# Performance work log

Measured on AMD Instinct MI355X. Metric: run time of the kernel, lower is better.

## Reference

```python
import jax, jax.numpy as jnp
import numpy as np

ROPE_THETA = 10000.0
NUM_HEADS = 16


def _apply_rope(t, positions):
    # t: [B, H, S, dh]; positions: [S] int
    dh = t.shape[-1]
    inv_freq = 1.0 / (ROPE_THETA ** (jnp.arange(0, dh, 2, dtype=jnp.float32) / dh))  # [dh/2]
    ang = positions.astype(jnp.float32)[:, None] * inv_freq[None, :]  # [S, dh/2]
    cos = jnp.cos(ang)[None, None]  # [1,1,S,dh/2]
    sin = jnp.sin(ang)[None, None]
    t1 = t[..., 0::2]
    t2 = t[..., 1::2]
    r1 = t1 * cos - t2 * sin
    r2 = t1 * sin + t2 * cos
    # interleave back: (r1_0, r2_0, r1_1, r2_1, ...)
    return jnp.stack([r1, r2], axis=-1).reshape(t.shape)


def setup_inputs() -> dict:
    key = jax.random.key(0)
    ks = jax.random.split(key, 5)
    B, S, D = 4, 2048, 1024
    sigma = np.sqrt(2.0 / (D + D))
    return {
        "x": jax.random.normal(ks[0], (B, S, D), dtype=jnp.float32),
        "WQ": jax.random.normal(ks[1], (D, D), dtype=jnp.float32) * sigma,
        "WK": jax.random.normal(ks[2], (D, D), dtype=jnp.float32) * sigma,
        "WV": jax.random.normal(ks[3], (D, D), dtype=jnp.float32) * sigma,
        "WO": jax.random.normal(ks[4], (D, D), dtype=jnp.float32) * sigma,
        "token_positions": jnp.arange(S, dtype=jnp.int32),
    }


def reference(x, WQ, WK, WV, WO, token_positions):
    B, S, D = x.shape
    H = NUM_HEADS
    dh = D // H

    def proj(W):
        # x @ W.T, then split heads -> [B, H, S, dh]
        return jnp.einsum('bsd,ed->bse', x, W).reshape(B, S, H, dh).transpose(0, 2, 1, 3)

    Q = _apply_rope(proj(WQ), token_positions)
    K = _apply_rope(proj(WK), token_positions)
    V = proj(WV)

    scale = 1.0 / jnp.sqrt(jnp.asarray(dh, dtype=x.dtype))
    scores = jnp.einsum('bhqd,bhkd->bhqk', Q, K) * scale  # [B,H,S,S]
    causal = jnp.tril(jnp.ones((S, S), dtype=bool))
    scores = jnp.where(causal[None, None], scores, jnp.asarray(-jnp.inf, dtype=scores.dtype))
    attn = jax.nn.softmax(scores, axis=-1)
    out = jnp.einsum('bhqk,bhkd->bhqd', attn, V)  # [B,H,S,dh]
    out = out.transpose(0, 2, 1, 3).reshape(B, S, D)
    return out @ WO.T
```

## Files before the change

kernel.cpp:

```cpp
#include <hip/hip_runtime.h>
#include <hip/hip_bf16.h>
#include <math.h>

constexpr int NB   = 4;
constexpr int SEQ  = 2048;
constexpr int DM   = 1024;
constexpr int NH   = 16;
constexpr int DH2  = 64;
constexpr int NROWS = NB * SEQ;

typedef __attribute__((ext_vector_type(8))) short bf16x8;
typedef __attribute__((ext_vector_type(4))) short bf16x4;
typedef __attribute__((ext_vector_type(4))) float f32x4;

__device__ __forceinline__ unsigned short f2bf(float f) {
  __hip_bfloat16 h = __float2bfloat16(f);
  return *reinterpret_cast<unsigned short*>(&h);
}

__device__ __forceinline__ f32x4 mfma16(bf16x8 a, bf16x8 b, f32x4 c) {
  return __builtin_amdgcn_mfma_f32_16x16x32_bf16(a, b, c, 0, 0, 0);
}

__device__ __forceinline__ f32x4 mfma16k16(bf16x4 a, bf16x4 b, f32x4 c) {
  asm("v_mfma_f32_16x16x16_bf16 %0, %1, %2, %0" : "+v"(c) : "v"(a), "v"(b));
  return c;
}

__device__ __forceinline__ void gload_lds16(const void* g, void* l) {
  __builtin_amdgcn_global_load_lds(
      (const __attribute__((address_space(1))) void*)g,
      (__attribute__((address_space(3))) void*)l, 16, 0, 0);
}

__global__ void cast_kernel(const float* __restrict__ in,
                            unsigned short* __restrict__ out, int n4) {
  int i = blockIdx.x * blockDim.x + threadIdx.x;
  int stride = gridDim.x * blockDim.x;
  for (int idx = i; idx < n4; idx += stride) {
    float4 v = reinterpret_cast<const float4*>(in)[idx];
    ushort4 o;
    o.x = f2bf(v.x); o.y = f2bf(v.y); o.z = f2bf(v.z); o.w = f2bf(v.w);
    reinterpret_cast<ushort4*>(out)[idx] = o;
  }
}

__global__ void cast4_kernel(const float* __restrict__ w0, const float* __restrict__ w1,
                             const float* __restrict__ w2, const float* __restrict__ w3,
                             unsigned short* __restrict__ out) {
  constexpr int N4 = DM * DM / 4;
  int idx = blockIdx.x * blockDim.x + threadIdx.x;
  if (idx >= N4) return;
  const float* ins[4] = {w0, w1, w2, w3};
#pragma unroll
  for (int wi = 0; wi < 4; ++wi) {
    float4 v = reinterpret_cast<const float4*>(ins[wi])[idx];
    ushort4 o;
    o.x = f2bf(v.x); o.y = f2bf(v.y); o.z = f2bf(v.z); o.w = f2bf(v.w);
    reinterpret_cast<ushort4*>(out + (size_t)wi * DM * DM)[idx] = o;
  }
}

__global__ void rope_table_kernel(float2* __restrict__ tab, const int* __restrict__ pos) {
  int idx = blockIdx.x * blockDim.x + threadIdx.x;
  if (idx >= SEQ * 32) return;
  int s = idx >> 5, i = idx & 31;
  float inv = powf(10000.0f, -(float)i * (1.0f / 32.0f));
  float ang = (float)pos[s] * inv;
  tab[idx] = make_float2(cosf(ang), sinf(ang));
}

template<int MODE>
__global__ __launch_bounds__(256)
void gemm_bt(const unsigned short* __restrict__ Ag,
             const unsigned short* __restrict__ Bg,
             void* __restrict__ Cout,
             const float2* __restrict__ tab)
{
  constexpr int K = DM;
  __shared__ unsigned short As[128 * 32];
  __shared__ unsigned short Bs[128 * 32];
  const int tid = threadIdx.x;
  const int w = tid >> 6, lane = tid & 63;
  const int wr = w >> 1, wc = w & 1;
  const int r = lane & 15, g = lane >> 4;
  const int rowTile = blockIdx.x, colTile = blockIdx.y;
  const unsigned short* Abase = Ag + (size_t)rowTile * 128 * K;
  const unsigned short* Bbase = Bg + (size_t)colTile * 128 * K;

  f32x4 acc[4][4];
#pragma unroll
  for (int m = 0; m < 4; ++m)
#pragma unroll
    for (int n = 0; n < 4; ++n) acc[m][n] = f32x4{0.f, 0.f, 0.f, 0.f};

  const int e0 = w * 1024 + lane * 8;

  for (int k0 = 0; k0 < K; k0 += 32) {
#pragma unroll
    for (int c = 0; c < 2; ++c) {
      int e = e0 + c * 512;
      int trow = e >> 5, tcol = e & 31;
      gload_lds16(Abase + (size_t)trow * K + k0 + tcol, As + (w * 2 + c) * 512);
      gload_lds16(Bbase + (size_t)trow * K + k0 + tcol, Bs + (w * 2 + c) * 512);
    }
    __syncthreads();
    bf16x8 a[4], b[4];
#pragma unroll
    for (int m = 0; m < 4; ++m)
      a[m] = *reinterpret_cast<const bf16x8*>(As + (wr * 64 + m * 16 + r) * 32 + g * 8);
#pragma unroll
    for (int n = 0; n < 4; ++n)
      b[n] = *reinterpret_cast<const bf16x8*>(Bs + (wc * 64 + n * 16 + r) * 32 + g * 8);
#pragma unroll
    for (int m = 0; m < 4; ++m)
#pragma unroll
      for (int n = 0; n < 4; ++n)
        acc[m][n] = mfma16(a[m], b[n], acc[m][n]);
    __syncthreads();
  }

  const int row0 = rowTile * 128 + wr * 64;
  const int col0 = colTile * 128 + wc * 64;
  if constexpr (MODE == 0) {
    float* C = reinterpret_cast<float*>(Cout);
#pragma unroll
    for (int m = 0; m < 4; ++m)
#pragma unroll
      for (int n = 0; n < 4; ++n)
#pragma unroll
        for (int j = 0; j < 4; ++j) {
          int rr = row0 + m * 16 + g * 4 + j;
          int cc = col0 + n * 16 + r;
          C[(size_t)rr * DM + cc] = acc[m][n][j];
        }
  } else {
    unsigned short* Ob = reinterpret_cast<unsigned short*>(Cout);
#pragma unroll
    for (int m = 0; m < 4; ++m)
#pragma unroll
      for (int n = 0; n < 4; ++n)
#pragma unroll
        for (int j = 0; j < 4; ++j) {
          int rr = row0 + m * 16 + g * 4 + j;
          int ee = col0 + n * 16 + r;
          float val = acc[m][n][j];
          if constexpr (MODE == 1) {
            float partner = __shfl_xor(val, 1);
            int dd = ee & 63;
            int sr = rr & (SEQ - 1);
            float2 cs = tab[sr * 32 + (dd >> 1)];
            val = val * cs.x + (((ee & 1) == 0) ? -partner : partner) * cs.y;
          }
          int bb = rr >> 11;
          int sr2 = rr & (SEQ - 1);
          int h = ee >> 6, d = ee & 63;
          Ob[((size_t)(bb * NH + h) * SEQ + sr2) * DH2 + d] = f2bf(val);
        }
  }
}

__global__ __launch_bounds__(256)
void flash_attn(const unsigned short* __restrict__ Qb,
                const unsigned short* __restrict__ Kb,
                const unsigned short* __restrict__ Vb,
                unsigned short* __restrict__ AO)
{
  constexpr int VST = 68;
  __shared__ unsigned short Kl[2 * 64 * 64];
  __shared__ unsigned short Vt[2][64 * VST];
  const int tid = threadIdx.x;
  const int w = tid >> 6, lane = tid & 63;
  const int r = lane & 15, g = lane >> 4;
  const int pr = blockIdx.x;
  const int bh = blockIdx.y;
  const unsigned short* Qh = Qb + (size_t)bh * SEQ * DH2;
  const unsigned short* Kh = Kb + (size_t)bh * SEQ * DH2;
  const unsigned short* Vh = Vb + (size_t)bh * SEQ * DH2;
  const int bb = bh >> 4, h = bh & 15;
  const int vd  = (lane & 7) * 8;
  const int vkv = w * 16 + (lane >> 3) * 2;
  const float C = 0.18033688f;
  const float M0 = 11.5415603f;
  const float NEG_INF = -__builtin_inff();

  const int krow   = tid >> 3;
  const int kcol16 = (tid & 7) ^ (krow & 7);
  const int kgoff  = krow * 64 + kcol16 * 8;
  const int kread0 = r * 64 + ((g ^ (r & 7)) * 8);
  const int kread1 = r * 64 + (((4 ^ g) ^ (r & 7)) * 8);

  for (int ctx = 0; ctx < 2; ++ctx) {
    const int qt = ctx ? pr : (15 - pr);
    const int q0w = qt * 128 + w * 32;
    const int nT  = 2 * qt + 2;
    const int myT = 2 * qt + 1 + (w >> 1);

    bf16x8 qf[2][2];
#pragma unroll
    for (int mq = 0; mq < 2; ++mq)
#pragma unroll
      for (int kk = 0; kk < 2; ++kk)
        qf[mq][kk] = *reinterpret_cast<const bf16x8*>(
            Qh + (size_t)(q0w + mq * 16 + r) * DH2 + kk * 32 + g * 8);

    gload_lds16(Kh + kgoff, Kl + w * 512);
    gload_lds16(Kh + kgoff + 2048, Kl + 2048 + w * 512);
    {
      uint4 a0 = *reinterpret_cast<const uint4*>(Vh + (size_t)vkv * DH2 + vd);
      uint4 a1 = *reinterpret_cast<const uint4*>(Vh + (size_t)(vkv + 1) * DH2 + vd);
      const unsigned int* d0 = reinterpret_cast<const unsigned int*>(&a0);
      const unsigned int* d1 = reinterpret_cast<const unsigned int*>(&a1);
#pragma unroll
      for (int k2 = 0; k2 < 4; ++k2) {
        *reinterpret_cast<unsigned int*>(&Vt[0][(vd + 2 * k2) * VST + vkv]) =
            __builtin_amdgcn_perm(d1[k2], d0[k2], 0x05040100u);
        *reinterpret_cast<unsigned int*>(&Vt[0][(vd + 2 * k2 + 1) * VST + vkv]) =
            __builtin_amdgcn_perm(d1[k2], d0[k2], 0x07060302u);
      }
    }
    __syncthreads();

    f32x4 oacc[2][4];
    float l_part[2];
#pragma unroll
    for (int mq = 0; mq < 2; ++mq) {
#pragma unroll
      for (int nd = 0; nd < 4; ++nd) oacc[mq][nd] = f32x4{0.f, 0.f, 0.f, 0.f};
      l_part[mq] = 0.f;
    }

    uint4 va0, va1;
    for (int t = 0; t < nT; ++t) {
      const int cur = t & 1;
      const unsigned short* Klp = Kl + (cur ? 4096 : 0);
      unsigned short* Kln = Kl + (cur ? 0 : 4096);
      const bool haveNext = (t + 1 < nT);

      if (haveNext) {
        const size_t kv0n = (size_t)(t + 1) * 64;
        gload_lds16(Kh + kv0n * 64 + kgoff, Kln + w * 512);
        gload_lds16(Kh + kv0n * 64 + kgoff + 2048, Kln + 2048 + w * 512);
        va0 = *reinterpret_cast<const uint4*>(Vh + (kv0n + vkv) * DH2 + vd);
        va1 = *reinterpret_cast<const uint4*>(Vh + (kv0n + vkv + 1) * DH2 + vd);
      }

      if (t < myT) {
        const int kv0 = t * 64;
        bf16x8 kf0[4], kf1[4];
#pragma unroll
        for (int nk = 0; nk < 4; ++nk) {
          kf0[nk] = *reinterpret_cast<const bf16x8*>(Klp + kread0 + nk * 1024);
          kf1[nk] = *reinterpret_cast<const bf16x8*>(Klp + kread1 + nk * 1024);
        }
        f32x4 sacc[2][4];
#pragma unroll
        for (int mq = 0; mq < 2; ++mq)
#pragma unroll
          for (int nk = 0; nk < 4; ++nk) sacc[mq][nk] = f32x4{0.f, 0.f, 0.f, 0.f};
        __builtin_amdgcn_s_setprio(1);
#pragma unroll
        for (int mq = 0; mq < 2; ++mq)
#pragma unroll
          for (int nk = 0; nk < 4; ++nk)
            sacc[mq][nk] = mfma16(kf0[nk], qf[mq][0], sacc[mq][nk]);
#pragma unroll
        for (int mq = 0; mq < 2; ++mq)
#pragma unroll
          for (int nk = 0; nk < 4; ++nk)
            sacc[mq][nk] = mfma16(kf1[nk], qf[mq][1], sacc[mq][nk]);
        __builtin_amdgcn_s_setprio(0);

        if (t == myT - 1) {
#pragma unroll
          for (int mq = 0; mq < 2; ++mq) {
            const int qg = q0w + mq * 16 + r;
#pragma unroll
            for (int nk = 0; nk < 4; ++nk)
#pragma unroll
              for (int j = 0; j < 4; ++j) {
                int kg = kv0 + nk * 16 + g * 4 + j;
                if (kg > qg) sacc[mq][nk][j] = NEG_INF;
              }
          }
        }

        bf16x4 pa[2][4];
#pragma unroll
        for (int mq = 0; mq < 2; ++mq) {
          float ls = 0.f;
#pragma unroll
          for (int nk = 0; nk < 4; ++nk) {
            float p0 = __builtin_amdgcn_exp2f(fmaf(sacc[mq][nk][0], C, -M0));
            float p1 = __builtin_amdgcn_exp2f(fmaf(sacc[mq][nk][1], C, -M0));
            float p2 = __builtin_amdgcn_exp2f(fmaf(sacc[mq][nk][2], C, -M0));
            float p3 = __builtin_amdgcn_exp2f(fmaf(sacc[mq][nk][3], C, -M0));
            ls += (p0 + p1) + (p2 + p3);
            pa[mq][nk] = bf16x4{(short)f2bf(p0), (short)f2bf(p1),
                                (short)f2bf(p2), (short)f2bf(p3)};
          }
          l_part[mq] += ls;
        }

        __builtin_amdgcn_s_setprio(1);
#pragma unroll
        for (int nd = 0; nd < 4; ++nd) {
          bf16x4 vb[4];
#pragma unroll
          for (int nk = 0; nk < 4; ++nk)
            vb[nk] = *reinterpret_cast<const bf16x4*>(
                &Vt[cur][(nd * 16 + r) * VST + nk * 16 + 4 * g]);
#pragma unroll
          for (int mq = 0; mq < 2; ++mq)
#pragma unroll
            for (int nk = 0; nk < 4; ++nk)
              oacc[mq][nd] = mfma16k16(pa[mq][nk], vb[nk], oacc[mq][nd]);
        }
        __builtin_amdgcn_s_setprio(0);
      }

      if (haveNext) {
        const unsigned int* d0 = reinterpret_cast<const unsigned int*>(&va0);
        const unsigned int* d1 = reinterpret_cast<const unsigned int*>(&va1);
#pragma unroll
        for (int k2 = 0; k2 < 4; ++k2) {
          *reinterpret_cast<unsigned int*>(&Vt[cur ^ 1][(vd + 2 * k2) * VST + vkv]) =
              __builtin_amdgcn_perm(d1[k2], d0[k2], 0x05040100u);
          *reinterpret_cast<unsigned int*>(&Vt[cur ^ 1][(vd + 2 * k2 + 1) * VST + vkv]) =
              __builtin_amdgcn_perm(d1[k2], d0[k2], 0x07060302u);
        }
      }
      __syncthreads();
    }

#pragma unroll
    for (int mq = 0; mq < 2; ++mq) {
      float l = l_part[mq];
      l += __shfl_xor(l, 16);
      l += __shfl_xor(l, 32);
#pragma unroll
      for (int j = 0; j < 4; ++j) {
        float inv = 1.0f / __shfl(l, g * 4 + j);
        int srow = q0w + mq * 16 + g * 4 + j;
#pragma unroll
        for (int nd = 0; nd < 4; ++nd) {
          int d = nd * 16 + r;
          AO[(size_t)(bb * SEQ + srow) * DM + h * DH2 + d] = f2bf(oacc[mq][nd][j] * inv);
        }
      }
    }
  }
}

extern "C" void kernel_launch(void* const* d_in, const int* in_sizes, int n_in,
                              void* d_out, int out_size, void* d_ws, size_t ws_size,
                              hipStream_t stream) {
  const float* x  = (const float*)d_in[0];
  const float* WQ = (const float*)d_in[1];
  const float* WK = (const float*)d_in[2];
  const float* WV = (const float*)d_in[3];
  const float* WO = (const float*)d_in[4];
  const int* pos  = (const int*)d_in[5];

  char* ws = (char*)d_ws;
  unsigned short* xb  = (unsigned short*)(ws + 0);
  unsigned short* wqb = (unsigned short*)(ws + (16u << 20));
  unsigned short* wkb = (unsigned short*)(ws + (18u << 20));
  unsigned short* wvb = (unsigned short*)(ws + (20u << 20));
  unsigned short* wob = (unsigned short*)(ws + (22u << 20));
  unsigned short* Qb  = (unsigned short*)(ws + (24u << 20));
  unsigned short* Kb  = (unsigned short*)(ws + (40u << 20));
  unsigned short* Vb  = (unsigned short*)(ws + (56u << 20));
  unsigned short* AO  = (unsigned short*)(ws + (72u << 20));
  float2* tab = (float2*)(ws + (88u << 20));

  cast_kernel<<<2048, 256, 0, stream>>>(x, xb, NROWS * DM / 4);
  cast4_kernel<<<DM * DM / 4 / 256, 256, 0, stream>>>(WQ, WK, WV, WO, wqb);
  rope_table_kernel<<<(SEQ * 32 + 255) / 256, 256, 0, stream>>>(tab, pos);

  dim3 gproj(NROWS / 128, DM / 128);
  gemm_bt<1><<<gproj, 256, 0, stream>>>(xb, wqb, (void*)Qb, tab);
  gemm_bt<1><<<gproj, 256, 0, stream>>>(xb, wkb, (void*)Kb, tab);
  gemm_bt<2><<<gproj, 256, 0, stream>>>(xb, wvb, (void*)Vb, nullptr);
  flash_attn<<<dim3(8, NB * NH), 256, 0, stream>>>(Qb, Kb, Vb, AO);
  gemm_bt<0><<<gproj, 256, 0, stream>>>(AO, wob, d_out, nullptr);
}
```

Measured before the change: 195.7 us.

## Double-buffer GEMM LDS tiles and widen flash-attention KV tiles to 128

```diff
diff --git a/kernel.cpp b/kernel.cpp
--- a/kernel.cpp
+++ b/kernel.cpp
@@ -78,8 +78,8 @@
              const float2* __restrict__ tab)
 {
   constexpr int K = DM;
-  __shared__ unsigned short As[128 * 32];
-  __shared__ unsigned short Bs[128 * 32];
+  __shared__ unsigned short As[2][128 * 32];
+  __shared__ unsigned short Bs[2][128 * 32];
   const int tid = threadIdx.x;
   const int w = tid >> 6, lane = tid & 63;
   const int wr = w >> 1, wc = w & 1;
@@ -95,29 +95,38 @@
     for (int n = 0; n < 4; ++n) acc[m][n] = f32x4{0.f, 0.f, 0.f, 0.f};
 
   const int e0 = w * 1024 + lane * 8;
-
-  for (int k0 = 0; k0 < K; k0 += 32) {
-#pragma unroll
-    for (int c = 0; c < 2; ++c) {
-      int e = e0 + c * 512;
-      int trow = e >> 5, tcol = e & 31;
-      gload_lds16(Abase + (size_t)trow * K + k0 + tcol, As + (w * 2 + c) * 512);
-      gload_lds16(Bbase + (size_t)trow * K + k0 + tcol, Bs + (w * 2 + c) * 512);
-    }
-    __syncthreads();
+  const int trow0 = e0 >> 5,           tcol0 = e0 & 31;
+  const int trow1 = (e0 + 512) >> 5,   tcol1 = (e0 + 512) & 31;
+
+  gload_lds16(Abase + (size_t)trow0 * K + tcol0, &As[0][0] + (w * 2 + 0) * 512);
+  gload_lds16(Bbase + (size_t)trow0 * K + tcol0, &Bs[0][0] + (w * 2 + 0) * 512);
+  gload_lds16(Abase + (size_t)trow1 * K + tcol1, &As[0][0] + (w * 2 + 1) * 512);
+  gload_lds16(Bbase + (size_t)trow1 * K + tcol1, &Bs[0][0] + (w * 2 + 1) * 512);
+  __syncthreads();
+
+  int cur = 0;
+  for (int t = 0; t < K / 32; ++t) {
+    if (t + 1 < K / 32) {
+      const int k1 = (t + 1) * 32;
+      gload_lds16(Abase + (size_t)trow0 * K + k1 + tcol0, &As[cur ^ 1][0] + (w * 2 + 0) * 512);
+      gload_lds16(Bbase + (size_t)trow0 * K + k1 + tcol0, &Bs[cur ^ 1][0] + (w * 2 + 0) * 512);
+      gload_lds16(Abase + (size_t)trow1 * K + k1 + tcol1, &As[cur ^ 1][0] + (w * 2 + 1) * 512);
+      gload_lds16(Bbase + (size_t)trow1 * K + k1 + tcol1, &Bs[cur ^ 1][0] + (w * 2 + 1) * 512);
+    }
     bf16x8 a[4], b[4];
 #pragma unroll
     for (int m = 0; m < 4; ++m)
-      a[m] = *reinterpret_cast<const bf16x8*>(As + (wr * 64 + m * 16 + r) * 32 + g * 8);
+      a[m] = *reinterpret_cast<const bf16x8*>(&As[cur][0] + (wr * 64 + m * 16 + r) * 32 + g * 8);
 #pragma unroll
     for (int n = 0; n < 4; ++n)
-      b[n] = *reinterpret_cast<const bf16x8*>(Bs + (wc * 64 + n * 16 + r) * 32 + g * 8);
+      b[n] = *reinterpret_cast<const bf16x8*>(&Bs[cur][0] + (wc * 64 + n * 16 + r) * 32 + g * 8);
 #pragma unroll
     for (int m = 0; m < 4; ++m)
 #pragma unroll
       for (int n = 0; n < 4; ++n)
         acc[m][n] = mfma16(a[m], b[n], acc[m][n]);
     __syncthreads();
+    cur ^= 1;
   }
 
   const int row0 = rowTile * 128 + wr * 64;
@@ -166,8 +175,8 @@
                 const unsigned short* __restrict__ Vb,
                 unsigned short* __restrict__ AO)
 {
-  constexpr int VST = 68;
-  __shared__ unsigned short Kl[2 * 64 * 64];
+  constexpr int VST = 132;
+  __shared__ unsigned short Kl[2][128 * 64];
   __shared__ unsigned short Vt[2][64 * VST];
   const int tid = threadIdx.x;
   const int w = tid >> 6, lane = tid & 63;
@@ -178,23 +187,21 @@
   const unsigned short* Kh = Kb + (size_t)bh * SEQ * DH2;
   const unsigned short* Vh = Vb + (size_t)bh * SEQ * DH2;
   const int bb = bh >> 4, h = bh & 15;
-  const int vd  = (lane & 7) * 8;
-  const int vkv = w * 16 + (lane >> 3) * 2;
   const float C = 0.18033688f;
   const float M0 = 11.5415603f;
   const float NEG_INF = -__builtin_inff();
 
-  const int krow   = tid >> 3;
-  const int kcol16 = (tid & 7) ^ (krow & 7);
-  const int kgoff  = krow * 64 + kcol16 * 8;
+  const int krow = tid >> 3;
+  const int kgo  = krow * 64 + ((tid & 7) ^ (krow & 7)) * 8;
   const int kread0 = r * 64 + ((g ^ (r & 7)) * 8);
   const int kread1 = r * 64 + (((4 ^ g) ^ (r & 7)) * 8);
+  const int vd  = (lane & 7) * 8;
+  const int vkv = w * 16 + (lane >> 3) * 2;
 
   for (int ctx = 0; ctx < 2; ++ctx) {
     const int qt = ctx ? pr : (15 - pr);
     const int q0w = qt * 128 + w * 32;
-    const int nT  = 2 * qt + 2;
-    const int myT = 2 * qt + 1 + (w >> 1);
+    const int nT  = qt + 1;
 
     bf16x8 qf[2][2];
 #pragma unroll
@@ -204,18 +211,24 @@
         qf[mq][kk] = *reinterpret_cast<const bf16x8*>(
             Qh + (size_t)(q0w + mq * 16 + r) * DH2 + kk * 32 + g * 8);
 
-    gload_lds16(Kh + kgoff, Kl + w * 512);
-    gload_lds16(Kh + kgoff + 2048, Kl + 2048 + w * 512);
     {
-      uint4 a0 = *reinterpret_cast<const uint4*>(Vh + (size_t)vkv * DH2 + vd);
-      uint4 a1 = *reinterpret_cast<const uint4*>(Vh + (size_t)(vkv + 1) * DH2 + vd);
+      const unsigned short* ks = Kh + kgo;
+      unsigned short* kd = &Kl[0][0] + w * 512;
+#pragma unroll
+      for (int ro = 0; ro < 4; ++ro)
+        gload_lds16(ks + ro * 2048, kd + ro * 2048);
+    }
+#pragma unroll
+    for (int hf = 0; hf < 2; ++hf) {
+      uint4 a0 = *reinterpret_cast<const uint4*>(Vh + (size_t)(hf * 64 + vkv) * DH2 + vd);
+      uint4 a1 = *reinterpret_cast<const uint4*>(Vh + (size_t)(hf * 64 + vkv + 1) * DH2 + vd);
       const unsigned int* d0 = reinterpret_cast<const unsigned int*>(&a0);
       const unsigned int* d1 = reinterpret_cast<const unsigned int*>(&a1);
 #pragma unroll
       for (int k2 = 0; k2 < 4; ++k2) {
-        *reinterpret_cast<unsigned int*>(&Vt[0][(vd + 2 * k2) * VST + vkv]) =
+        *reinterpret_cast<unsigned int*>(&Vt[0][(vd + 2 * k2) * VST + hf * 64 + vkv]) =
             __builtin_amdgcn_perm(d1[k2], d0[k2], 0x05040100u);
-        *reinterpret_cast<unsigned int*>(&Vt[0][(vd + 2 * k2 + 1) * VST + vkv]) =
+        *reinterpret_cast<unsigned int*>(&Vt[0][(vd + 2 * k2 + 1) * VST + hf * 64 + vkv]) =
             __builtin_amdgcn_perm(d1[k2], d0[k2], 0x07060302u);
       }
     }
@@ -230,91 +243,96 @@
       l_part[mq] = 0.f;
     }
 
-    uint4 va0, va1;
+    uint4 va0, va1, va2, va3;
     for (int t = 0; t < nT; ++t) {
       const int cur = t & 1;
-      const unsigned short* Klp = Kl + (cur ? 4096 : 0);
-      unsigned short* Kln = Kl + (cur ? 0 : 4096);
       const bool haveNext = (t + 1 < nT);
 
       if (haveNext) {
-        const size_t kv0n = (size_t)(t + 1) * 64;
-        gload_lds16(Kh + kv0n * 64 + kgoff, Kln + w * 512);
-        gload_lds16(Kh + kv0n * 64 + kgoff + 2048, Kln + 2048 + w * 512);
+        const size_t kv0n = (size_t)(t + 1) * 128;
+        const unsigned short* ks = Kh + kv0n * 64 + kgo;
+        unsigned short* kd = &Kl[cur ^ 1][0] + w * 512;
+#pragma unroll
+        for (int ro = 0; ro < 4; ++ro)
+          gload_lds16(ks + ro * 2048, kd + ro * 2048);
         va0 = *reinterpret_cast<const uint4*>(Vh + (kv0n + vkv) * DH2 + vd);
         va1 = *reinterpret_cast<const uint4*>(Vh + (kv0n + vkv + 1) * DH2 + vd);
+        va2 = *reinterpret_cast<const uint4*>(Vh + (kv0n + 64 + vkv) * DH2 + vd);
+        va3 = *reinterpret_cast<const uint4*>(Vh + (kv0n + 64 + vkv + 1) * DH2 + vd);
       }
 
-      if (t < myT) {
-        const int kv0 = t * 64;
-        bf16x8 kf0[4], kf1[4];
-#pragma unroll
-        for (int nk = 0; nk < 4; ++nk) {
-          kf0[nk] = *reinterpret_cast<const bf16x8*>(Klp + kread0 + nk * 1024);
-          kf1[nk] = *reinterpret_cast<const bf16x8*>(Klp + kread1 + nk * 1024);
-        }
-        f32x4 sacc[2][4];
+      {
+        const int kv0 = t * 128;
+        const unsigned short* Klp = &Kl[cur][0];
+        const bool diag = (t == nT - 1);
+        const int nkb = diag ? (2 * w + 2) : 8;
+
+        f32x4 sacc[2][8];
 #pragma unroll
         for (int mq = 0; mq < 2; ++mq)
 #pragma unroll
-          for (int nk = 0; nk < 4; ++nk) sacc[mq][nk] = f32x4{0.f, 0.f, 0.f, 0.f};
+          for (int nk = 0; nk < 8; ++nk) sacc[mq][nk] = f32x4{0.f, 0.f, 0.f, 0.f};
         __builtin_amdgcn_s_setprio(1);
 #pragma unroll
-        for (int mq = 0; mq < 2; ++mq)
-#pragma unroll
-          for (int nk = 0; nk < 4; ++nk)
-            sacc[mq][nk] = mfma16(kf0[nk], qf[mq][0], sacc[mq][nk]);
-#pragma unroll
-        for (int mq = 0; mq < 2; ++mq)
-#pragma unroll
-          for (int nk = 0; nk < 4; ++nk)
-            sacc[mq][nk] = mfma16(kf1[nk], qf[mq][1], sacc[mq][nk]);
+        for (int kk = 0; kk < 2; ++kk) {
+          const int kr = (kk == 0) ? kread0 : kread1;
+          bf16x8 kf[8];
+#pragma unroll
+          for (int nk = 0; nk < 8; ++nk)
+            kf[nk] = *reinterpret_cast<const bf16x8*>(Klp + kr + nk * 1024);
+#pragma unroll
+          for (int mq = 0; mq < 2; ++mq)
+#pragma unroll
+            for (int nk = 0; nk < 8; ++nk)
+              sacc[mq][nk] = mfma16(kf[nk], qf[mq][kk], sacc[mq][nk]);
+        }
         __builtin_amdgcn_s_setprio(0);
 
-        if (t == myT - 1) {
+        if (diag) {
 #pragma unroll
           for (int mq = 0; mq < 2; ++mq) {
             const int qg = q0w + mq * 16 + r;
 #pragma unroll
-            for (int nk = 0; nk < 4; ++nk)
-#pragma unroll
-              for (int j = 0; j < 4; ++j) {
-                int kg = kv0 + nk * 16 + g * 4 + j;
-                if (kg > qg) sacc[mq][nk][j] = NEG_INF;
-              }
+            for (int nk = 0; nk < 8; ++nk)
+              if (nk < nkb)
+#pragma unroll
+                for (int j = 0; j < 4; ++j) {
+                  int kg = kv0 + nk * 16 + g * 4 + j;
+                  if (kg > qg) sacc[mq][nk][j] = NEG_INF;
+                }
           }
         }
 
-        bf16x4 pa[2][4];
+        bf16x4 pa[2][8];
 #pragma unroll
         for (int mq = 0; mq < 2; ++mq) {
           float ls = 0.f;
 #pragma unroll
-          for (int nk = 0; nk < 4; ++nk) {
-            float p0 = __builtin_amdgcn_exp2f(fmaf(sacc[mq][nk][0], C, -M0));
-            float p1 = __builtin_amdgcn_exp2f(fmaf(sacc[mq][nk][1], C, -M0));
-            float p2 = __builtin_amdgcn_exp2f(fmaf(sacc[mq][nk][2], C, -M0));
-            float p3 = __builtin_amdgcn_exp2f(fmaf(sacc[mq][nk][3], C, -M0));
-            ls += (p0 + p1) + (p2 + p3);
-            pa[mq][nk] = bf16x4{(short)f2bf(p0), (short)f2bf(p1),
-                                (short)f2bf(p2), (short)f2bf(p3)};
-          }
+          for (int nk = 0; nk < 8; ++nk)
+            if (nk < nkb) {
+              float p0 = __builtin_amdgcn_exp2f(fmaf(sacc[mq][nk][0], C, -M0));
+              float p1 = __builtin_amdgcn_exp2f(fmaf(sacc[mq][nk][1], C, -M0));
+              float p2 = __builtin_amdgcn_exp2f(fmaf(sacc[mq][nk][2], C, -M0));
+              float p3 = __builtin_amdgcn_exp2f(fmaf(sacc[mq][nk][3], C, -M0));
+              ls += (p0 + p1) + (p2 + p3);
+              pa[mq][nk] = bf16x4{(short)f2bf(p0), (short)f2bf(p1),
+                                  (short)f2bf(p2), (short)f2bf(p3)};
+            }
           l_part[mq] += ls;
         }
 
         __builtin_amdgcn_s_setprio(1);
 #pragma unroll
         for (int nd = 0; nd < 4; ++nd) {
-          bf16x4 vb[4];
-#pragma unroll
-          for (int nk = 0; nk < 4; ++nk)
-            vb[nk] = *reinterpret_cast<const bf16x4*>(
-                &Vt[cur][(nd * 16 + r) * VST + nk * 16 + 4 * g]);
-#pragma unroll
-          for (int mq = 0; mq < 2; ++mq)
-#pragma unroll
-            for (int nk = 0; nk < 4; ++nk)
-              oacc[mq][nd] = mfma16k16(pa[mq][nk], vb[nk], oacc[mq][nd]);
+#pragma unroll
+          for (int nk = 0; nk < 8; ++nk)
+            if (nk < nkb) {
+              bf16x4 vb = *reinterpret_cast<const bf16x4*>(
+                  &Vt[cur][(nd * 16 + r) * VST + nk * 16 + 4 * g]);
+#pragma unroll
+              for (int mq = 0; mq < 2; ++mq)
+                oacc[mq][nd] = mfma16k16(pa[mq][nk], vb, oacc[mq][nd]);
+            }
         }
         __builtin_amdgcn_s_setprio(0);
       }
@@ -322,12 +340,18 @@
       if (haveNext) {
         const unsigned int* d0 = reinterpret_cast<const unsigned int*>(&va0);
         const unsigned int* d1 = reinterpret_cast<const unsigned int*>(&va1);
+        const unsigned int* d2 = reinterpret_cast<const unsigned int*>(&va2);
+        const unsigned int* d3 = reinterpret_cast<const unsigned int*>(&va3);
 #pragma unroll
         for (int k2 = 0; k2 < 4; ++k2) {
           *reinterpret_cast<unsigned int*>(&Vt[cur ^ 1][(vd + 2 * k2) * VST + vkv]) =
               __builtin_amdgcn_perm(d1[k2], d0[k2], 0x05040100u);
           *reinterpret_cast<unsigned int*>(&Vt[cur ^ 1][(vd + 2 * k2 + 1) * VST + vkv]) =
               __builtin_amdgcn_perm(d1[k2], d0[k2], 0x07060302u);
+          *reinterpret_cast<unsigned int*>(&Vt[cur ^ 1][(vd + 2 * k2) * VST + 64 + vkv]) =
+              __builtin_amdgcn_perm(d3[k2], d2[k2], 0x05040100u);
+          *reinterpret_cast<unsigned int*>(&Vt[cur ^ 1][(vd + 2 * k2 + 1) * VST + 64 + vkv]) =
+              __builtin_amdgcn_perm(d3[k2], d2[k2], 0x07060302u);
         }
       }
       __syncthreads();
```

Result: slower. 237.1 us (+21.1%).

## Fuse Q/K/V projections into one 768-thread GEMM sharing the x tile

Applied to the files above, without the earlier changes.

```diff
diff --git a/kernel.cpp b/kernel.cpp
--- a/kernel.cpp
+++ b/kernel.cpp
@@ -70,12 +70,87 @@
   tab[idx] = make_float2(cosf(ang), sinf(ang));
 }
 
-template<int MODE>
+__global__ __launch_bounds__(768)
+void gemm_qkv3(const unsigned short* __restrict__ Ag,
+               const unsigned short* __restrict__ Wg,
+               unsigned short* __restrict__ Qb,
+               unsigned short* __restrict__ Kb,
+               unsigned short* __restrict__ Vb,
+               const float2* __restrict__ tab)
+{
+  constexpr int K = DM;
+  __shared__ unsigned short S[4][128 * 32];
+  const int tid = threadIdx.x;
+  const int w = tid >> 6, lane = tid & 63;
+  const int wv = w >> 2;
+  const int wr = (w >> 1) & 1, wc = w & 1;
+  const int r = lane & 15, g = lane >> 4;
+  const int rowTile = blockIdx.x, colTile = blockIdx.y;
+  const unsigned short* Abase = Ag + (size_t)rowTile * 128 * K;
+  const unsigned short* Wbase = Wg + (size_t)colTile * 128 * K;
+
+  f32x4 acc[4][4];
+#pragma unroll
+  for (int m = 0; m < 4; ++m)
+#pragma unroll
+    for (int n = 0; n < 4; ++n) acc[m][n] = f32x4{0.f, 0.f, 0.f, 0.f};
+
+  const int srow = lane >> 2, scol = (lane & 3) * 8;
+
+  for (int k0 = 0; k0 < K; k0 += 32) {
+    for (int c = w; c < 32; c += 12) {
+      const int p = c >> 3, pr = (c & 7) * 16;
+      const unsigned short* base =
+          (p == 0) ? Abase : (Wbase + (size_t)(p - 1) * DM * DM);
+      gload_lds16(base + (size_t)(pr + srow) * K + k0 + scol, &S[0][0] + c * 512);
+    }
+    __syncthreads();
+    bf16x8 a[4], b[4];
+#pragma unroll
+    for (int m = 0; m < 4; ++m)
+      a[m] = *reinterpret_cast<const bf16x8*>(&S[0][0] + (wr * 64 + m * 16 + r) * 32 + g * 8);
+#pragma unroll
+    for (int n = 0; n < 4; ++n)
+      b[n] = *reinterpret_cast<const bf16x8*>(&S[1 + wv][0] + (wc * 64 + n * 16 + r) * 32 + g * 8);
+#pragma unroll
+    for (int m = 0; m < 4; ++m)
+#pragma unroll
+      for (int n = 0; n < 4; ++n)
+        acc[m][n] = mfma16(a[m], b[n], acc[m][n]);
+    __syncthreads();
+  }
+
+  unsigned short* Ob = (wv == 0) ? Qb : (wv == 1) ? Kb : Vb;
+  const bool doRope = (wv < 2);
+  const int row0 = rowTile * 128 + wr * 64;
+  const int col0 = colTile * 128 + wc * 64;
+#pragma unroll
+  for (int m = 0; m < 4; ++m)
+#pragma unroll
+    for (int n = 0; n < 4; ++n)
+#pragma unroll
+      for (int j = 0; j < 4; ++j) {
+        int rr = row0 + m * 16 + g * 4 + j;
+        int ee = col0 + n * 16 + r;
+        float val = acc[m][n][j];
+        if (doRope) {
+          float partner = __shfl_xor(val, 1);
+          int dd = ee & 63;
+          int sr = rr & (SEQ - 1);
+          float2 cs = tab[sr * 32 + (dd >> 1)];
+          val = val * cs.x + (((ee & 1) == 0) ? -partner : partner) * cs.y;
+        }
+        int bb = rr >> 11;
+        int sr2 = rr & (SEQ - 1);
+        int h = ee >> 6, d = ee & 63;
+        Ob[((size_t)(bb * NH + h) * SEQ + sr2) * DH2 + d] = f2bf(val);
+      }
+}
+
 __global__ __launch_bounds__(256)
-void gemm_bt(const unsigned short* __restrict__ Ag,
-             const unsigned short* __restrict__ Bg,
-             void* __restrict__ Cout,
-             const float2* __restrict__ tab)
+void gemm_bt0(const unsigned short* __restrict__ Ag,
+              const unsigned short* __restrict__ Bg,
+              float* __restrict__ C)
 {
   constexpr int K = DM;
   __shared__ unsigned short As[128 * 32];
@@ -122,42 +197,16 @@
 
   const int row0 = rowTile * 128 + wr * 64;
   const int col0 = colTile * 128 + wc * 64;
-  if constexpr (MODE == 0) {
-    float* C = reinterpret_cast<float*>(Cout);
-#pragma unroll
-    for (int m = 0; m < 4; ++m)
-#pragma unroll
-      for (int n = 0; n < 4; ++n)
-#pragma unroll
-        for (int j = 0; j < 4; ++j) {
-          int rr = row0 + m * 16 + g * 4 + j;
-          int cc = col0 + n * 16 + r;
-          C[(size_t)rr * DM + cc] = acc[m][n][j];
-        }
-  } else {
-    unsigned short* Ob = reinterpret_cast<unsigned short*>(Cout);
-#pragma unroll
-    for (int m = 0; m < 4; ++m)
-#pragma unroll
-      for (int n = 0; n < 4; ++n)
-#pragma unroll
-        for (int j = 0; j < 4; ++j) {
-          int rr = row0 + m * 16 + g * 4 + j;
-          int ee = col0 + n * 16 + r;
-          float val = acc[m][n][j];
-          if constexpr (MODE == 1) {
-            float partner = __shfl_xor(val, 1);
-            int dd = ee & 63;
-            int sr = rr & (SEQ - 1);
-            float2 cs = tab[sr * 32 + (dd >> 1)];
-            val = val * cs.x + (((ee & 1) == 0) ? -partner : partner) * cs.y;
-          }
-          int bb = rr >> 11;
-          int sr2 = rr & (SEQ - 1);
-          int h = ee >> 6, d = ee & 63;
-          Ob[((size_t)(bb * NH + h) * SEQ + sr2) * DH2 + d] = f2bf(val);
-        }
-  }
+#pragma unroll
+  for (int m = 0; m < 4; ++m)
+#pragma unroll
+    for (int n = 0; n < 4; ++n)
+#pragma unroll
+      for (int j = 0; j < 4; ++j) {
+        int rr = row0 + m * 16 + g * 4 + j;
+        int cc = col0 + n * 16 + r;
+        C[(size_t)rr * DM + cc] = acc[m][n][j];
+      }
 }
 
 __global__ __launch_bounds__(256)
@@ -365,8 +414,6 @@
   char* ws = (char*)d_ws;
   unsigned short* xb  = (unsigned short*)(ws + 0);
   unsigned short* wqb = (unsigned short*)(ws + (16u << 20));
-  unsigned short* wkb = (unsigned short*)(ws + (18u << 20));
-  unsigned short* wvb = (unsigned short*)(ws + (20u << 20));
   unsigned short* wob = (unsigned short*)(ws + (22u << 20));
   unsigned short* Qb  = (unsigned short*)(ws + (24u << 20));
   unsigned short* Kb  = (unsigned short*)(ws + (40u << 20));
@@ -378,10 +425,7 @@
   cast4_kernel<<<DM * DM / 4 / 256, 256, 0, stream>>>(WQ, WK, WV, WO, wqb);
   rope_table_kernel<<<(SEQ * 32 + 255) / 256, 256, 0, stream>>>(tab, pos);
 
-  dim3 gproj(NROWS / 128, DM / 128);
-  gemm_bt<1><<<gproj, 256, 0, stream>>>(xb, wqb, (void*)Qb, tab);
-  gemm_bt<1><<<gproj, 256, 0, stream>>>(xb, wkb, (void*)Kb, tab);
-  gemm_bt<2><<<gproj, 256, 0, stream>>>(xb, wvb, (void*)Vb, nullptr);
+  gemm_qkv3<<<dim3(NROWS / 128, DM / 128), 768, 0, stream>>>(xb, wqb, Qb, Kb, Vb, tab);
   flash_attn<<<dim3(8, NB * NH), 256, 0, stream>>>(Qb, Kb, Vb, AO);
-  gemm_bt<0><<<gproj, 256, 0, stream>>>(AO, wob, d_out, nullptr);
-}
+  gemm_bt0<<<dim3(NROWS / 128, DM / 128), 256, 0, stream>>>(AO, wob, (float*)d_out);
+}
```

Measured after the change: 221.6 us. 13.2% more time.

## Process paired big and small query tiles in one shared KV sweep

Applied to the files above, without the earlier changes.

```diff
diff --git a/kernel.cpp b/kernel.cpp
--- a/kernel.cpp
+++ b/kernel.cpp
@@ -190,69 +190,86 @@
   const int kread0 = r * 64 + ((g ^ (r & 7)) * 8);
   const int kread1 = r * 64 + (((4 ^ g) ^ (r & 7)) * 8);
 
-  for (int ctx = 0; ctx < 2; ++ctx) {
-    const int qt = ctx ? pr : (15 - pr);
-    const int q0w = qt * 128 + w * 32;
-    const int nT  = 2 * qt + 2;
-    const int myT = 2 * qt + 1 + (w >> 1);
-
-    bf16x8 qf[2][2];
-#pragma unroll
-    for (int mq = 0; mq < 2; ++mq)
-#pragma unroll
-      for (int kk = 0; kk < 2; ++kk)
-        qf[mq][kk] = *reinterpret_cast<const bf16x8*>(
-            Qh + (size_t)(q0w + mq * 16 + r) * DH2 + kk * 32 + g * 8);
-
-    gload_lds16(Kh + kgoff, Kl + w * 512);
-    gload_lds16(Kh + kgoff + 2048, Kl + 2048 + w * 512);
-    {
-      uint4 a0 = *reinterpret_cast<const uint4*>(Vh + (size_t)vkv * DH2 + vd);
-      uint4 a1 = *reinterpret_cast<const uint4*>(Vh + (size_t)(vkv + 1) * DH2 + vd);
-      const unsigned int* d0 = reinterpret_cast<const unsigned int*>(&a0);
-      const unsigned int* d1 = reinterpret_cast<const unsigned int*>(&a1);
-#pragma unroll
-      for (int k2 = 0; k2 < 4; ++k2) {
-        *reinterpret_cast<unsigned int*>(&Vt[0][(vd + 2 * k2) * VST + vkv]) =
-            __builtin_amdgcn_perm(d1[k2], d0[k2], 0x05040100u);
-        *reinterpret_cast<unsigned int*>(&Vt[0][(vd + 2 * k2 + 1) * VST + vkv]) =
-            __builtin_amdgcn_perm(d1[k2], d0[k2], 0x07060302u);
+  const int qtB = 15 - pr, qtS = pr;
+  const int q0B = qtB * 128 + w * 32;
+  const int q0S = qtS * 128 + w * 32;
+  const int nTB  = 2 * qtB + 2;
+  const int myTB = 2 * qtB + 1 + (w >> 1);
+  const int myTS = 2 * qtS + 1 + (w >> 1);
+
+  bf16x8 qfB[2][2], qfS[2][2];
+#pragma unroll
+  for (int mq = 0; mq < 2; ++mq)
+#pragma unroll
+    for (int kk = 0; kk < 2; ++kk) {
+      qfB[mq][kk] = *reinterpret_cast<const bf16x8*>(
+          Qh + (size_t)(q0B + mq * 16 + r) * DH2 + kk * 32 + g * 8);
+      qfS[mq][kk] = *reinterpret_cast<const bf16x8*>(
+          Qh + (size_t)(q0S + mq * 16 + r) * DH2 + kk * 32 + g * 8);
+    }
+
+  gload_lds16(Kh + kgoff, Kl + w * 512);
+  gload_lds16(Kh + kgoff + 2048, Kl + 2048 + w * 512);
+  {
+    uint4 a0 = *reinterpret_cast<const uint4*>(Vh + (size_t)vkv * DH2 + vd);
+    uint4 a1 = *reinterpret_cast<const uint4*>(Vh + (size_t)(vkv + 1) * DH2 + vd);
+    const unsigned int* d0 = reinterpret_cast<const unsigned int*>(&a0);
+    const unsigned int* d1 = reinterpret_cast<const unsigned int*>(&a1);
+#pragma unroll
+    for (int k2 = 0; k2 < 4; ++k2) {
+      *reinterpret_cast<unsigned int*>(&Vt[0][(vd + 2 * k2) * VST + vkv]) =
+          __builtin_amdgcn_perm(d1[k2], d0[k2], 0x05040100u);
+      *reinterpret_cast<unsigned int*>(&Vt[0][(vd + 2 * k2 + 1) * VST + vkv]) =
+          __builtin_amdgcn_perm(d1[k2], d0[k2], 0x07060302u);
+    }
+  }
+  __syncthreads();
+
+  f32x4 oaccB[2][4], oaccS[2][4];
+  float lB[2], lS[2];
+#pragma unroll
+  for (int mq = 0; mq < 2; ++mq) {
+#pragma unroll
+    for (int nd = 0; nd < 4; ++nd) {
+      oaccB[mq][nd] = f32x4{0.f, 0.f, 0.f, 0.f};
+      oaccS[mq][nd] = f32x4{0.f, 0.f, 0.f, 0.f};
+    }
+    lB[mq] = 0.f;
+    lS[mq] = 0.f;
+  }
+
+  uint4 va0, va1;
+  for (int t = 0; t < nTB; ++t) {
+    const int cur = t & 1;
+    const unsigned short* Klp = Kl + (cur ? 4096 : 0);
+    unsigned short* Kln = Kl + (cur ? 0 : 4096);
+    const bool haveNext = (t + 1 < nTB);
+
+    if (haveNext) {
+      const size_t kv0n = (size_t)(t + 1) * 64;
+      gload_lds16(Kh + kv0n * 64 + kgoff, Kln + w * 512);
+      gload_lds16(Kh + kv0n * 64 + kgoff + 2048, Kln + 2048 + w * 512);
+      va0 = *reinterpret_cast<const uint4*>(Vh + (kv0n + vkv) * DH2 + vd);
+      va1 = *reinterpret_cast<const uint4*>(Vh + (kv0n + vkv + 1) * DH2 + vd);
+    }
+
+    if (t < myTB) {
+      const int kv0 = t * 64;
+      bf16x8 kf0[4], kf1[4];
+#pragma unroll
+      for (int nk = 0; nk < 4; ++nk) {
+        kf0[nk] = *reinterpret_cast<const bf16x8*>(Klp + kread0 + nk * 1024);
+        kf1[nk] = *reinterpret_cast<const bf16x8*>(Klp + kread1 + nk * 1024);
       }
-    }
-    __syncthreads();
-
-    f32x4 oacc[2][4];
-    float l_part[2];
-#pragma unroll
-    for (int mq = 0; mq < 2; ++mq) {
-#pragma unroll
-      for (int nd = 0; nd < 4; ++nd) oacc[mq][nd] = f32x4{0.f, 0.f, 0.f, 0.f};
-      l_part[mq] = 0.f;
-    }
-
-    uint4 va0, va1;
-    for (int t = 0; t < nT; ++t) {
-      const int cur = t & 1;
-      const unsigned short* Klp = Kl + (cur ? 4096 : 0);
-      unsigned short* Kln = Kl + (cur ? 0 : 4096);
-      const bool haveNext = (t + 1 < nT);
-
-      if (haveNext) {
-        const size_t kv0n = (size_t)(t + 1) * 64;
-        gload_lds16(Kh + kv0n * 64 + kgoff, Kln + w * 512);
-        gload_lds16(Kh + kv0n * 64 + kgoff + 2048, Kln + 2048 + w * 512);
-        va0 = *reinterpret_cast<const uint4*>(Vh + (kv0n + vkv) * DH2 + vd);
-        va1 = *reinterpret_cast<const uint4*>(Vh + (kv0n + vkv + 1) * DH2 + vd);
-      }
-
-      if (t < myT) {
-        const int kv0 = t * 64;
-        bf16x8 kf0[4], kf1[4];
-#pragma unroll
-        for (int nk = 0; nk < 4; ++nk) {
-          kf0[nk] = *reinterpret_cast<const bf16x8*>(Klp + kread0 + nk * 1024);
-          kf1[nk] = *reinterpret_cast<const bf16x8*>(Klp + kread1 + nk * 1024);
-        }
+      bf16x4 vb[4][4];
+#pragma unroll
+      for (int nd = 0; nd < 4; ++nd)
+#pragma unroll
+        for (int nk = 0; nk < 4; ++nk)
+          vb[nd][nk] = *reinterpret_cast<const bf16x4*>(
+              &Vt[cur][(nd * 16 + r) * VST + nk * 16 + 4 * g]);
+
+      {
         f32x4 sacc[2][4];
 #pragma unroll
         for (int mq = 0; mq < 2; ++mq)
@@ -263,18 +280,18 @@
         for (int mq = 0; mq < 2; ++mq)
 #pragma unroll
           for (int nk = 0; nk < 4; ++nk)
-            sacc[mq][nk] = mfma16(kf0[nk], qf[mq][0], sacc[mq][nk]);
+            sacc[mq][nk] = mfma16(kf0[nk], qfB[mq][0], sacc[mq][nk]);
 #pragma unroll
         for (int mq = 0; mq < 2; ++mq)
 #pragma unroll
           for (int nk = 0; nk < 4; ++nk)
-            sacc[mq][nk] = mfma16(kf1[nk], qf[mq][1], sacc[mq][nk]);
+            sacc[mq][nk] = mfma16(kf1[nk], qfB[mq][1], sacc[mq][nk]);
         __builtin_amdgcn_s_setprio(0);
 
-        if (t == myT - 1) {
+        if (t == myTB - 1) {
 #pragma unroll
           for (int mq = 0; mq < 2; ++mq) {
-            const int qg = q0w + mq * 16 + r;
+            const int qg = q0B + mq * 16 + r;
 #pragma unroll
             for (int nk = 0; nk < 4; ++nk)
 #pragma unroll
@@ -299,53 +316,113 @@
             pa[mq][nk] = bf16x4{(short)f2bf(p0), (short)f2bf(p1),
                                 (short)f2bf(p2), (short)f2bf(p3)};
           }
-          l_part[mq] += ls;
+          lB[mq] += ls;
         }
 
         __builtin_amdgcn_s_setprio(1);
 #pragma unroll
-        for (int nd = 0; nd < 4; ++nd) {
-          bf16x4 vb[4];
-#pragma unroll
-          for (int nk = 0; nk < 4; ++nk)
-            vb[nk] = *reinterpret_cast<const bf16x4*>(
-                &Vt[cur][(nd * 16 + r) * VST + nk * 16 + 4 * g]);
+        for (int nd = 0; nd < 4; ++nd)
 #pragma unroll
           for (int mq = 0; mq < 2; ++mq)
 #pragma unroll
             for (int nk = 0; nk < 4; ++nk)
-              oacc[mq][nd] = mfma16k16(pa[mq][nk], vb[nk], oacc[mq][nd]);
-        }
+              oaccB[mq][nd] = mfma16k16(pa[mq][nk], vb[nd][nk], oaccB[mq][nd]);
         __builtin_amdgcn_s_setprio(0);
       }
 
-      if (haveNext) {
-        const unsigned int* d0 = reinterpret_cast<const unsigned int*>(&va0);
-        const unsigned int* d1 = reinterpret_cast<const unsigned int*>(&va1);
-#pragma unroll
-        for (int k2 = 0; k2 < 4; ++k2) {
-          *reinterpret_cast<unsigned int*>(&Vt[cur ^ 1][(vd + 2 * k2) * VST + vkv]) =
-              __builtin_amdgcn_perm(d1[k2], d0[k2], 0x05040100u);
-          *reinterpret_cast<unsigned int*>(&Vt[cur ^ 1][(vd + 2 * k2 + 1) * VST + vkv]) =
-              __builtin_amdgcn_perm(d1[k2], d0[k2], 0x07060302u);
-        }
+      if (t < myTS) {
+        f32x4 sacc[2][4];
+#pragma unroll
+        for (int mq = 0; mq < 2; ++mq)
+#pragma unroll
+          for (int nk = 0; nk < 4; ++nk) sacc[mq][nk] = f32x4{0.f, 0.f, 0.f, 0.f};
+        __builtin_amdgcn_s_setprio(1);
+#pragma unroll
+        for (int mq = 0; mq < 2; ++mq)
+#pragma unroll
+          for (int nk = 0; nk < 4; ++nk)
+            sacc[mq][nk] = mfma16(kf0[nk], qfS[mq][0], sacc[mq][nk]);
+#pragma unroll
+        for (int mq = 0; mq < 2; ++mq)
+#pragma unroll
+          for (int nk = 0; nk < 4; ++nk)
+            sacc[mq][nk] = mfma16(kf1[nk], qfS[mq][1], sacc[mq][nk]);
+        __builtin_amdgcn_s_setprio(0);
+
+        if (t == myTS - 1) {
+#pragma unroll
+          for (int mq = 0; mq < 2; ++mq) {
+            const int qg = q0S + mq * 16 + r;
+#pragma unroll
+            for (int nk = 0; nk < 4; ++nk)
+#pragma unroll
+              for (int j = 0; j < 4; ++j) {
+                int kg = kv0 + nk * 16 + g * 4 + j;
+                if (kg > qg) sacc[mq][nk][j] = NEG_INF;
+              }
+          }
+        }
+
+        bf16x4 pa[2][4];
+#pragma unroll
+        for (int mq = 0; mq < 2; ++mq) {
+          float ls = 0.f;
+#pragma unroll
+          for (int nk = 0; nk < 4; ++nk) {
+            float p0 = __builtin_amdgcn_exp2f(fmaf(sacc[mq][nk][0], C, -M0));
+            float p1 = __builtin_amdgcn_exp2f(fmaf(sacc[mq][nk][1], C, -M0));
+            float p2 = __builtin_amdgcn_exp2f(fmaf(sacc[mq][nk][2], C, -M0));
+            float p3 = __builtin_amdgcn_exp2f(fmaf(sacc[mq][nk][3], C, -M0));
+            ls += (p0 + p1) + (p2 + p3);
+            pa[mq][nk] = bf16x4{(short)f2bf(p0), (short)f2bf(p1),
+                                (short)f2bf(p2), (short)f2bf(p3)};
+          }
+          lS[mq] += ls;
+        }
+
+        __builtin_amdgcn_s_setprio(1);
+#pragma unroll
+        for (int nd = 0; nd < 4; ++nd)
+#pragma unroll
+          for (int mq = 0; mq < 2; ++mq)
+#pragma unroll
+            for (int nk = 0; nk < 4; ++nk)
+              oaccS[mq][nd] = mfma16k16(pa[mq][nk], vb[nd][nk], oaccS[mq][nd]);
+        __builtin_amdgcn_s_setprio(0);
       }
-      __syncthreads();
-    }
-
+    }
+
+    if (haveNext) {
+      const unsigned int* d0 = reinterpret_cast<const unsigned int*>(&va0);
+      const unsigned int* d1 = reinterpret_cast<const unsigned int*>(&va1);
+#pragma unroll
+      for (int k2 = 0; k2 < 4; ++k2) {
+        *reinterpret_cast<unsigned int*>(&Vt[cur ^ 1][(vd + 2 * k2) * VST + vkv]) =
+            __builtin_amdgcn_perm(d1[k2], d0[k2], 0x05040100u);
+        *reinterpret_cast<unsigned int*>(&Vt[cur ^ 1][(vd + 2 * k2 + 1) * VST + vkv]) =
+            __builtin_amdgcn_perm(d1[k2], d0[k2], 0x07060302u);
+      }
+    }
+    __syncthreads();
+  }
+
+#pragma unroll
+  for (int half = 0; half < 2; ++half) {
+    const int q0 = half ? q0S : q0B;
 #pragma unroll
     for (int mq = 0; mq < 2; ++mq) {
-      float l = l_part[mq];
+      float l = half ? lS[mq] : lB[mq];
       l += __shfl_xor(l, 16);
       l += __shfl_xor(l, 32);
 #pragma unroll
       for (int j = 0; j < 4; ++j) {
         float inv = 1.0f / __shfl(l, g * 4 + j);
-        int srow = q0w + mq * 16 + g * 4 + j;
+        int srow = q0 + mq * 16 + g * 4 + j;
 #pragma unroll
         for (int nd = 0; nd < 4; ++nd) {
           int d = nd * 16 + r;
-          AO[(size_t)(bb * SEQ + srow) * DM + h * DH2 + d] = f2bf(oacc[mq][nd][j] * inv);
+          f32x4 o = half ? oaccS[mq][nd] : oaccB[mq][nd];
+          AO[(size_t)(bb * SEQ + srow) * DM + h * DH2 + d] = f2bf(o[j] * inv);
         }
       }
     }
```

New measurement: 222.8 us. 1.14x slower.
